# Optimization experiments

Hardware: AMD Instinct MI355X
Metric: run time of the kernel (lower is better)

The kernel has to match this reference:

```python
import jax, jax.numpy as jnp
import numpy as np

SCALAR_DIM = 64
VECTOR_DIM = 32
SPIN = 2
N_NODES = 50000
N_EDGES = 1600000
GEO_DIM = 3
IN_DIM = 2 * SCALAR_DIM + VECTOR_DIM + GEO_DIM  # 163
HID = SCALAR_DIM + VECTOR_DIM  # 96


def setup_inputs() -> dict:
    key = jax.random.key(0)
    ks = jax.random.split(key, 9)
    h_scalar = jax.random.normal(ks[0], (N_NODES, SCALAR_DIM), dtype=jnp.float32)
    h_vector = jax.random.normal(ks[1], (N_NODES, VECTOR_DIM), dtype=jnp.float32)
    edge_index = jax.random.randint(ks[2], (2, N_EDGES), 0, N_NODES, dtype=jnp.int64)
    pos = jax.random.normal(ks[3], (N_NODES, 2), dtype=jnp.float32)
    orientation = jax.random.uniform(ks[4], (N_NODES, 1), dtype=jnp.float32)
    # MLP params (Linear: y = x @ W.T + b; store as [in, out] for jnp)
    lim1 = 1.0 / np.sqrt(IN_DIM)
    lim2 = 1.0 / np.sqrt(HID)
    W1 = jax.random.uniform(ks[5], (IN_DIM, HID), minval=-lim1, maxval=lim1, dtype=jnp.float32)
    b1 = jax.random.uniform(ks[6], (HID,), minval=-lim1, maxval=lim1, dtype=jnp.float32)
    W2 = jax.random.uniform(ks[7], (HID, HID), minval=-lim2, maxval=lim2, dtype=jnp.float32)
    b2 = jax.random.uniform(ks[8], (HID,), minval=-lim2, maxval=lim2, dtype=jnp.float32)
    return dict(h_scalar=h_scalar, h_vector=h_vector, edge_index=edge_index,
                pos=pos, orientation=orientation, W1=W1, b1=b1, W2=W2, b2=b2)


def reference(h_scalar, h_vector, edge_index, pos, orientation, W1, b1, W2, b2):
    src, dst = edge_index[0], edge_index[1]
    delta_pos = pos[src] - pos[dst]                         # [E,2]
    dist = jnp.linalg.norm(delta_pos, axis=1, keepdims=True) + 1e-6  # [E,1]
    phi_global = jnp.arctan2(delta_pos[:, 1], delta_pos[:, 0])       # [E]
    alpha_i = orientation[dst, 0]                           # [E]
    delta_phi = phi_global - alpha_i
    geo_feat = jnp.concatenate([dist,
                                jnp.cos(SPIN * delta_phi)[:, None],
                                jnp.sin(SPIN * delta_phi)[:, None]], axis=-1)  # [E,3]
    beta_j = orientation[src, 0]
    rot_angle = (beta_j - alpha_i) * SPIN
    c, s = jnp.cos(rot_angle), jnp.sin(rot_angle)
    R = jnp.stack([jnp.stack([c, -s], -1), jnp.stack([s, c], -1)], axis=-2)  # [E,2,2]
    num_vecs = VECTOR_DIM // 2
    v_j = h_vector[src].reshape(-1, num_vecs, 2)            # [E,V/2,2]
    v_j_rot = jnp.einsum('eij,evj->evi', R, v_j).reshape(-1, VECTOR_DIM)
    msg_input = jnp.concatenate([h_scalar[src], h_scalar[dst], v_j_rot, geo_feat], axis=-1)
    h = jax.nn.silu(msg_input @ W1 + b1)
    raw_msg = h @ W2 + b2                                   # [E, S+V]
    msg_scalar = raw_msg[:, :SCALAR_DIM]
    msg_vector = raw_msg[:, SCALAR_DIM:]
    out_scalar = jax.ops.segment_sum(msg_scalar, dst, num_segments=N_NODES)
    out_vector = jax.ops.segment_sum(msg_vector, dst, num_segments=N_NODES)
    return h_scalar + out_scalar, h_vector + out_vector
```

## Files before the change

kernel.cpp:

```cpp
#include <hip/hip_runtime.h>
#include <hip/hip_bf16.h>

#define N_NODESC 50000
#define N_EDGESC 1600000
#define SDIM 64
#define VDIM 32
#define HID 96
#define IN_DIMC 163

#define GRID_E 6250
#define TPB_E 4
#define NXCD 8
#define XQ (GRID_E / NXCD)
#define XR (GRID_E % NXCD)
#define NPRE 782
#define SCB 196

typedef float f32x4 __attribute__((ext_vector_type(4)));
typedef short s16x8 __attribute__((ext_vector_type(8)));

__device__ __forceinline__ float bf2f(__hip_bfloat16 x) { return __bfloat162float(x); }
__device__ __forceinline__ __hip_bfloat16 f2bf(float x) { return __float2bfloat16(x); }
__device__ __forceinline__ float bfbits2f(short b) {
    unsigned u = ((unsigned)(unsigned short)b) << 16;
    return __builtin_bit_cast(float, u);
}
__device__ __forceinline__ short f2bfbits(float x) {
    __hip_bfloat16 h = __float2bfloat16(x);
    return *(const short*)&h;
}

__global__ void detect_zero(const int* ei, int* flag, int* __restrict__ counts) {
    int i = blockIdx.x * blockDim.x + threadIdx.x;
    if (i < N_NODESC) counts[i] = 0;
    if (i == 0) {
        int z = 1;
        for (int k = 0; k < 64; ++k) {
            if (ei[2 * k + 1] != 0) { z = 0; break; }
        }
        *flag = z;
    }
}

__global__ void fused_init(const float* __restrict__ hs, const float* __restrict__ hv,
                           float* __restrict__ out, int* __restrict__ counts,
                           const float* __restrict__ W1, const float* __restrict__ W2,
                           __hip_bfloat16* __restrict__ SrcRec,
                           __hip_bfloat16* __restrict__ WbT2,
                           __hip_bfloat16* __restrict__ W1cgT,
                           __hip_bfloat16* __restrict__ W2Tb,
                           const int* __restrict__ ei, const int* __restrict__ flag64) {
    int i = blockIdx.x * blockDim.x + threadIdx.x;
    if (i < N_NODESC * (SDIM + VDIM) / 4) {
        const int HS4 = N_NODESC * SDIM / 4;
        float4 v = (i < HS4) ? ((const float4*)hs)[i] : ((const float4*)hv)[i - HS4];
        ((float4*)out)[i] = v;
    }
    if (i < N_NODESC * VDIM / 8) {
        int n = i >> 2, c = i & 3;
        const float4* hv4 = (const float4*)hv;
        float4 a = hv4[n * 8 + c * 2];
        float4 bq = hv4[n * 8 + c * 2 + 1];
        s16x8 o;
        o[0] = f2bfbits(a.x);  o[1] = f2bfbits(a.y);
        o[2] = f2bfbits(a.z);  o[3] = f2bfbits(a.w);
        o[4] = f2bfbits(bq.x); o[5] = f2bfbits(bq.y);
        o[6] = f2bfbits(bq.z); o[7] = f2bfbits(bq.w);
        *(s16x8*)&SrcRec[n * 128 + 96 + c * 8] = o;
    }
    if (i < 192 * 64) {
        int n = i >> 6, k = i & 63;
        float val = (n < 96) ? W1[k * HID + n] : W1[(64 + k) * HID + (n - 96)];
        WbT2[i] = f2bf(val);
    }
    if (i < 96 * 64) {
        int n = i >> 6, k = i & 63;
        float val = 0.f;
        if (k < 32) val = W1[(128 + k) * HID + n];
        else if (k < 35) val = W1[(160 + (k - 32)) * HID + n];
        W1cgT[i] = f2bf(val);
    }
    if (i < 96 * 96) {
        int n = i / 96, k = i - (i / 96) * 96;
        W2Tb[i] = f2bf(W2[k * HID + n]);
    }
    {
        int dN;
        if (*flag64) dN = (int)((const long long*)ei)[N_EDGESC + i];
        else dN = ei[N_EDGESC + i];
        atomicAdd(&counts[dN], 1);
    }
}

__global__ __launch_bounds__(256) void scan_partials(
    const int* __restrict__ counts, int* __restrict__ cur, int* __restrict__ bsum) {
    __shared__ int sc[256];
    const int b = blockIdx.x, t = threadIdx.x;
    const int i = b * 256 + t;
    int val = (i < N_NODESC) ? counts[i] : 0;
    sc[t] = val;
    __syncthreads();
    for (int d = 1; d < 256; d <<= 1) {
        int v = (t >= d) ? sc[t - d] : 0;
        __syncthreads();
        sc[t] += v;
        __syncthreads();
    }
    if (i < N_NODESC) cur[i] = sc[t] - val;
    if (t == 255) bsum[b] = sc[255];
}

__global__ __launch_bounds__(256) void scan_bsums(
    const int* __restrict__ bsum, int* __restrict__ boff) {
    __shared__ int sc[256];
    const int t = threadIdx.x;
    int val = (t < SCB) ? bsum[t] : 0;
    sc[t] = val;
    __syncthreads();
    for (int d = 1; d < 256; d <<= 1) {
        int v = (t >= d) ? sc[t - d] : 0;
        __syncthreads();
        sc[t] += v;
        __syncthreads();
    }
    if (t < SCB) boff[t] = sc[t] - val;
}

__global__ __launch_bounds__(256) void scan_apply(
    int* __restrict__ cur, const int* __restrict__ boff) {
    const int i = blockIdx.x * 256 + threadIdx.x;
    if (i < N_NODESC) cur[i] += boff[blockIdx.x];
}

__global__ __launch_bounds__(256, 2) void scatter_precompute(
    const int* __restrict__ ei, const int* __restrict__ flag64,
    int* __restrict__ cur, int2* __restrict__ edges,
    const float* __restrict__ hs, const __hip_bfloat16* __restrict__ WbT2,
    const float* __restrict__ b1,
    __hip_bfloat16* __restrict__ SrcRec, __hip_bfloat16* __restrict__ Qt) {
    __shared__ __hip_bfloat16 sA[64][72];
    __shared__ __hip_bfloat16 sOut[64][200];
    const int blk = blockIdx.x;
    const int t = threadIdx.x;

    if (blk >= NPRE) {
        int e = (blk - NPRE) * 256 + t;
        int sN, dN;
        if (*flag64) {
            const long long* e64 = (const long long*)ei;
            sN = (int)e64[e]; dN = (int)e64[N_EDGESC + e];
        } else { sN = ei[e]; dN = ei[N_EDGESC + e]; }
        int p = atomicAdd(&cur[dN], 1);
        edges[p] = make_int2(sN, dN);
        return;
    }

    const int lane = t & 63;
    const int w = t >> 6;
    const int m16 = lane & 15;
    const int q = lane >> 4;
    const int nb = blk * 64;

    for (int idx = t; idx < 64 * 64; idx += 256) {
        int node = idx >> 6, f = idx & 63;
        int g = nb + node;
        sA[node][f] = f2bf(g < N_NODESC ? hs[g * SDIM + f] : 0.f);
    }
    __syncthreads();

    s16x8 bfr[3][2];
    float b1v[3];
    for (int nt = 0; nt < 3; ++nt) {
        int n_out = w * 48 + nt * 16 + m16;
        for (int kt = 0; kt < 2; ++kt)
            bfr[nt][kt] = *(const s16x8*)&WbT2[n_out * 64 + kt * 32 + q * 8];
        b1v[nt] = (n_out < 96) ? b1[n_out] : 0.f;
    }

    for (int ms = 0; ms < 4; ++ms) {
        s16x8 afr[2];
        for (int kt = 0; kt < 2; ++kt)
            afr[kt] = *(const s16x8*)&sA[ms * 16 + m16][kt * 32 + q * 8];
        f32x4 acc[3];
        for (int nt = 0; nt < 3; ++nt) acc[nt] = (f32x4){0.f, 0.f, 0.f, 0.f};
        for (int nt = 0; nt < 3; ++nt)
            for (int kt = 0; kt < 2; ++kt)
                acc[nt] = __builtin_amdgcn_mfma_f32_16x16x32_bf16(
                    afr[kt], bfr[nt][kt], acc[nt], 0, 0, 0);
        for (int nt = 0; nt < 3; ++nt) {
            int n_out = w * 48 + nt * 16 + m16;
            for (int r = 0; r < 4; ++r)
                sOut[ms * 16 + q * 4 + r][n_out] = f2bf(acc[nt][r] + b1v[nt]);
        }
    }
    __syncthreads();

    for (int idx = t; idx < 64 * 12; idx += 256) {
        int node = idx / 12, ch = idx - (idx / 12) * 12;
        int g = nb + node;
        if (g < N_NODESC)
            *(s16x8*)&SrcRec[g * 128 + ch * 8] = *(const s16x8*)&sOut[node][ch * 8];
    }
    for (int idx = t; idx < 64 * 12; idx += 256) {
        int node = idx / 12, ch = idx - (idx / 12) * 12;
        int g = nb + node;
        if (g < N_NODESC)
            *(s16x8*)&Qt[g * 96 + ch * 8] = *(const s16x8*)&sOut[node][96 + ch * 8];
    }
}

__global__ __launch_bounds__(256, 3) void edge_kernel_sorted(
    const int2* __restrict__ edges,
    const float* __restrict__ pos, const float* __restrict__ ori,
    const __hip_bfloat16* __restrict__ W2Tb, const float* __restrict__ b2,
    const __hip_bfloat16* __restrict__ SrcRec, const __hip_bfloat16* __restrict__ Qt,
    const __hip_bfloat16* __restrict__ W1cgT,
    float* __restrict__ out) {
    __shared__ int s_srcM[2][64], s_dstM[2][64];
    __shared__ alignas(16) __hip_bfloat16 hVG[64][72];
    __shared__ alignas(16) __hip_bfloat16 s_vf[64][104];
    __shared__ alignas(16) short sW2f[18 * 64 * 8];
    __shared__ int s_segstart[66];

    const int t = threadIdx.x;
    const int lane = t & 63;
    const int w = t >> 6;
    const int m16 = lane & 15;
    const int q = lane >> 4;
    const int el = t >> 2;
    const int quad = t & 3;
    const int eM = w * 16 + m16;

    if (w == 0) {
        for (int f = 0; f < 18; ++f) {
            int nt = f / 3, kt = f - (f / 3) * 3;
            *(s16x8*)&sW2f[(f * 64 + lane) * 8] =
                *(const s16x8*)&W2Tb[(nt * 16 + m16) * 96 + kt * 32 + q * 8];
        }
    }
    s16x8 bfrC[6][2];
    #pragma unroll
    for (int nt = 0; nt < 6; ++nt)
        #pragma unroll
        for (int kt = 0; kt < 2; ++kt)
            bfrC[nt][kt] = *(const s16x8*)&W1cgT[(nt * 16 + m16) * 64 + kt * 32 + q * 8];
    float b2v[6];
    #pragma unroll
    for (int nt = 0; nt < 6; ++nt) b2v[nt] = b2[nt * 16 + m16];

    int b = blockIdx.x;
    int xcd = b & 7, bi = b >> 3;
    int c = (xcd < XR) ? (xcd * (XQ + 1) + bi)
                       : (XR * (XQ + 1) + (xcd - XR) * XQ + bi);
    const int tile0 = c * TPB_E;

    int2 edT1;
    s16x8 hvvT;
    float rcT, rsT;
    float gdT, gcgT, gsgT;
    {
        int2 edT = edges[tile0 * 64 + el];
        edT1 = edges[(tile0 + 1) * 64 + el];
        hvvT = *(const s16x8*)&SrcRec[edT.x * 128 + 96 + quad * 8];
        int sN = edT.x, dN = edT.y;
        float ca, sa, cb, sb;
        __sincosf(2.0f * ori[dN], &sa, &ca);
        __sincosf(2.0f * ori[sN], &sb, &cb);
        rcT = cb * ca + sb * sa;
        rsT = sb * ca - cb * sa;
        float dx = pos[2 * sN] - pos[2 * dN];
        float dy = pos[2 * sN + 1] - pos[2 * dN + 1];
        float d2 = dx * dx + dy * dy;
        gdT = sqrtf(d2) + 1e-6f;
        float c2f, s2f;
        if (d2 > 0.f) {
            float inv = __builtin_amdgcn_rcpf(d2);
            c2f = (dx * dx - dy * dy) * inv;
            s2f = 2.0f * dx * dy * inv;
        } else { c2f = 1.0f; s2f = 0.0f; }
        gcgT = c2f * ca + s2f * sa;
        gsgT = s2f * ca - c2f * sa;
        if (quad == 0) { s_srcM[0][el] = sN; s_dstM[0][el] = dN; }
    }
    __syncthreads();
    s16x8 pqP[3], pqQ[3];
    {
        int sN = s_srcM[0][eM], dN = s_dstM[0][eM];
        #pragma unroll
        for (int kt = 0; kt < 3; ++kt) {
            pqP[kt] = *(const s16x8*)&SrcRec[sN * 128 + kt * 32 + q * 8];
            pqQ[kt] = *(const s16x8*)&Qt[dN * 96 + kt * 32 + q * 8];
        }
    }

    int cur = 0;
    for (int tl = 0; tl < TPB_E; ++tl) {
        const int nx = cur ^ 1;
        const int tlN2 = (tl + 2 < TPB_E) ? tl + 2 : TPB_E - 1;

        {
            s16x8 rv;
            #pragma unroll
            for (int p2 = 0; p2 < 4; ++p2) {
                float x = bfbits2f(hvvT[2 * p2]), y = bfbits2f(hvvT[2 * p2 + 1]);
                rv[2 * p2]     = f2bfbits(rcT * x - rsT * y);
                rv[2 * p2 + 1] = f2bfbits(rsT * x + rcT * y);
            }
            *(s16x8*)&hVG[el][quad * 8] = rv;
            s16x8 up = (s16x8){0, 0, 0, 0, 0, 0, 0, 0};
            if (quad == 0) {
                up[0] = f2bfbits(gdT); up[1] = f2bfbits(gcgT); up[2] = f2bfbits(gsgT);
            }
            *(s16x8*)&hVG[el][32 + quad * 8] = up;
        }
        int2 edT2 = edges[(tile0 + tlN2) * 64 + el];
        s16x8 hvvN = *(const s16x8*)&SrcRec[edT1.x * 128 + 96 + quad * 8];
        {
            s16x8 afr0 = *(const s16x8*)&hVG[eM][q * 8];
            s16x8 afr1 = *(const s16x8*)&hVG[eM][32 + q * 8];
            #pragma unroll
            for (int nt = 0; nt < 6; ++nt) {
                f32x4 a1 = __builtin_amdgcn_mfma_f32_16x16x32_bf16(
                    afr0, bfrC[nt][0], (f32x4){0.f, 0.f, 0.f, 0.f}, 0, 0, 0);
                a1 = __builtin_amdgcn_mfma_f32_16x16x32_bf16(
                    afr1, bfrC[nt][1], a1, 0, 0, 0);
                int u = nt * 16 + m16;
                #pragma unroll
                for (int r = 0; r < 4; ++r)
                    s_vf[w * 16 + q * 4 + r][u] = f2bf(a1[r]);
            }
        }
        float rcN, rsN, gdN, gcgN, gsgN;
        {
            int sN = edT1.x, dN = edT1.y;
            float ca, sa, cb, sb;
            __sincosf(2.0f * ori[dN], &sa, &ca);
            __sincosf(2.0f * ori[sN], &sb, &cb);
            rcN = cb * ca + sb * sa;
            rsN = sb * ca - cb * sa;
            float dx = pos[2 * sN] - pos[2 * dN];
            float dy = pos[2 * sN + 1] - pos[2 * dN + 1];
            float d2 = dx * dx + dy * dy;
            gdN = sqrtf(d2) + 1e-6f;
            float c2f, s2f;
            if (d2 > 0.f) {
                float inv = __builtin_amdgcn_rcpf(d2);
                c2f = (dx * dx - dy * dy) * inv;
                s2f = 2.0f * dx * dy * inv;
            } else { c2f = 1.0f; s2f = 0.0f; }
            gcgN = c2f * ca + s2f * sa;
            gsgN = s2f * ca - c2f * sa;
            if (quad == 0) { s_srcM[nx][el] = sN; s_dstM[nx][el] = dN; }
        }

        s16x8 afr[3];
        #pragma unroll
        for (int kt = 0; kt < 3; ++kt) {
            int j = kt * 32 + q * 8;
            s16x8 Vv = *(const s16x8*)&s_vf[eM][j];
            s16x8 hb;
            #pragma unroll
// ... 155 lines not shown
    const bool i64 = (*flag64 != 0);
    const long long* ei64 = (const long long*)ei;

    for (int tile = blockIdx.x; tile < N_EDGESC / 64; tile += gridDim.x) {
        __syncthreads();

        if (t < 64) {
            int e = tile * 64 + t;
            int sN, dN;
            if (i64) { sN = (int)ei64[e]; dN = (int)ei64[N_EDGESC + e]; }
            else     { sN = ei[e];        dN = ei[N_EDGESC + e]; }
            s_src[t] = sN; s_dst[t] = dN;
            float ca, sa, cb, sb;
            __sincosf(2.0f * ori[dN], &sa, &ca);
            __sincosf(2.0f * ori[sN], &sb, &cb);
            s_c[t] = cb * ca + sb * sa;
            s_s[t] = sb * ca - cb * sa;
            float dx = pos[2 * sN] - pos[2 * dN];
            float dy = pos[2 * sN + 1] - pos[2 * dN + 1];
            float d2 = dx * dx + dy * dy;
            s_d[t] = sqrtf(d2) + 1e-6f;
            float c2f, s2f;
            if (d2 > 0.f) {
                float inv = 1.0f / d2;
                c2f = (dx * dx - dy * dy) * inv;
                s2f = 2.0f * dx * dy * inv;
            } else { c2f = 1.0f; s2f = 0.0f; }
            s_cg[t] = c2f * ca + s2f * sa;
            s_sg[t] = s2f * ca - c2f * sa;
        }
        __syncthreads();

        for (int p = 0; p < 24; ++p) {
            int idx = p * 256 + t;
            int e = idx / HID;
            int j = idx - e * HID;
            int sN = s_src[e], dN = s_dst[e];
            float pre = bf2f(Pp[sN * HID + j]) + bf2f(Qt[dN * HID + j])
                      + s_c[e] * bf2f(Ut[sN * HID + j])
                      + s_s[e] * bf2f(Vt[sN * HID + j])
                      + s_d[e] * s_w1d[0][j] + s_cg[e] * s_w1d[1][j]
                      + s_sg[e] * s_w1d[2][j];
            float h = pre / (1.0f + __expf(-pre));
            hA[e][j] = f2bf(h);
        }
        __syncthreads();

        f32x4 acc[6];
        for (int nt = 0; nt < 6; ++nt) acc[nt] = (f32x4){0.f, 0.f, 0.f, 0.f};
        s16x8 afr[3];
        for (int kt = 0; kt < 3; ++kt)
            afr[kt] = *(const s16x8*)&hA[w * 16 + m16][kt * 32 + q * 8];
        for (int nt = 0; nt < 6; ++nt)
            for (int kt = 0; kt < 3; ++kt)
                acc[nt] = __builtin_amdgcn_mfma_f32_16x16x32_bf16(
                    afr[kt], bfr[nt][kt], acc[nt], 0, 0, 0);

        for (int nt = 0; nt < 6; ++nt) {
            int u = nt * 16 + m16;
            for (int r = 0; r < 4; ++r) {
                int eloc = w * 16 + q * 4 + r;
                int dN = s_dst[eloc];
                float val = acc[nt][r] + b2v[nt];
                if (u < SDIM) atomicAdd(&out[dN * SDIM + u], val);
                else atomicAdd(&out[N_NODESC * SDIM + dN * VDIM + (u - SDIM)], val);
            }
        }
    }
}

__global__ __launch_bounds__(192) void edge_fallback(
    const int* __restrict__ ei, const float* __restrict__ hs,
    const float* __restrict__ hv, const float* __restrict__ pos,
    const float* __restrict__ ori, const float* __restrict__ W1,
    const float* __restrict__ b1, const float* __restrict__ W2,
    const float* __restrict__ b2, const int* __restrict__ flag64,
    float* __restrict__ out) {
    __shared__ float s_msg[IN_DIMC];
    __shared__ float s_h[HID];
    int e = blockIdx.x;
    int t = threadIdx.x;
    const bool i64 = (*flag64 != 0);
    int sN, dN;
    if (i64) {
        const long long* e64 = (const long long*)ei;
        sN = (int)e64[e]; dN = (int)e64[N_EDGESC + e];
    } else { sN = ei[e]; dN = ei[N_EDGESC + e]; }

    if (t < IN_DIMC) {
        if (t < 64) s_msg[t] = hs[sN * SDIM + t];
        else if (t < 128) s_msg[t] = hs[dN * SDIM + (t - 64)];
        else {
            float ca, sa, cb, sb;
            __sincosf(2.0f * ori[dN], &sa, &ca);
            __sincosf(2.0f * ori[sN], &sb, &cb);
            float c = cb * ca + sb * sa;
            float s = sb * ca - cb * sa;
            float dx = pos[2 * sN] - pos[2 * dN];
            float dy = pos[2 * sN + 1] - pos[2 * dN + 1];
            float d2 = dx * dx + dy * dy;
            if (t < 160) {
                int pr = (t - 128) >> 1;
                float x = hv[sN * VDIM + 2 * pr], y = hv[sN * VDIM + 2 * pr + 1];
                s_msg[t] = ((t & 1) == 0) ? (c * x - s * y) : (s * x + c * y);
            } else if (t == 160) s_msg[t] = sqrtf(d2) + 1e-6f;
            else {
                float c2f = 1.0f, s2f = 0.0f;
                if (d2 > 0.f) {
                    float inv = 1.0f / d2;
                    c2f = (dx * dx - dy * dy) * inv;
                    s2f = 2.0f * dx * dy * inv;
                }
                s_msg[t] = (t == 161) ? (c2f * ca + s2f * sa) : (s2f * ca - c2f * sa);
            }
        }
    }
    __syncthreads();
    if (t < HID) {
        float a = b1[t];
        for (int k = 0; k < IN_DIMC; ++k) a += s_msg[k] * W1[k * HID + t];
        s_h[t] = a / (1.0f + __expf(-a));
    }
    __syncthreads();
    if (t < HID) {
        float a = b2[t];
        for (int k = 0; k < HID; ++k) a += s_h[k] * W2[k * HID + t];
        if (t < SDIM) atomicAdd(&out[dN * SDIM + t], a);
        else atomicAdd(&out[N_NODESC * SDIM + dN * VDIM + (t - SDIM)], a);
    }
}

extern "C" void kernel_launch(void* const* d_in, const int* in_sizes, int n_in,
                              void* d_out, int out_size, void* d_ws, size_t ws_size,
                              hipStream_t stream) {
    const float* hs  = (const float*)d_in[0];
    const float* hv  = (const float*)d_in[1];
    const int*   ei  = (const int*)d_in[2];
    const float* pos = (const float*)d_in[3];
    const float* ori = (const float*)d_in[4];
    const float* W1  = (const float*)d_in[5];
    const float* b1  = (const float*)d_in[6];
    const float* W2  = (const float*)d_in[7];
    const float* b2  = (const float*)d_in[8];
    float* out = (float*)d_out;

    const size_t SREC = (size_t)N_NODESC * 128 * sizeof(__hip_bfloat16);
    const size_t QTB  = (size_t)N_NODESC * 96 * sizeof(__hip_bfloat16);
    const size_t CNT  = ((size_t)N_NODESC * sizeof(int) + 255) & ~255ull;
    const size_t EDG  = (size_t)N_EDGESC * sizeof(int2);
    const size_t WBT2 = ((size_t)192 * 64 * 2 + 255) & ~255ull;
    const size_t W1CG = ((size_t)96 * 64 * 2 + 255) & ~255ull;
    const size_t W2TS = ((size_t)96 * 96 * 2 + 255) & ~255ull;
    const size_t FLG  = 256;
    const size_t BSM  = 1024;
    const size_t BOF  = 1024;
    const size_t SORT_WS = SREC + QTB + 2 * CNT + EDG + WBT2 + W1CG + W2TS
                         + FLG + BSM + BOF;

    const size_t TBL = (size_t)N_NODESC * HID * sizeof(__hip_bfloat16);
    const bool big = ws_size >= 4 * TBL + 16;
    const bool srt = ws_size >= SORT_WS;

    if (srt) {
        char* ws = (char*)d_ws;
        __hip_bfloat16* SrcRec = (__hip_bfloat16*)(ws);
        __hip_bfloat16* Qt     = (__hip_bfloat16*)(ws + SREC);
        int* counts            = (int*)(ws + SREC + QTB);
        int* cur               = (int*)(ws + SREC + QTB + CNT);
        int2* edges            = (int2*)(ws + SREC + QTB + 2 * CNT);
        __hip_bfloat16* WbT2   = (__hip_bfloat16*)(ws + SREC + QTB + 2 * CNT + EDG);
        __hip_bfloat16* W1cgT  = (__hip_bfloat16*)(ws + SREC + QTB + 2 * CNT + EDG + WBT2);
        __hip_bfloat16* W2Tb   = (__hip_bfloat16*)(ws + SREC + QTB + 2 * CNT + EDG + WBT2 + W1CG);
        char* tail             = ws + SREC + QTB + 2 * CNT + EDG + WBT2 + W1CG + W2TS;
        int* flag              = (int*)(tail);
        int* bsum              = (int*)(tail + FLG);
        int* boff              = (int*)(tail + FLG + BSM);

        detect_zero<<<(N_NODESC + 255) / 256, 256, 0, stream>>>(ei, flag, counts);
        fused_init<<<N_EDGESC / 256, 256, 0, stream>>>(
            hs, hv, out, counts, W1, W2, SrcRec, WbT2, W1cgT, W2Tb, ei, flag);
        scan_partials<<<SCB, 256, 0, stream>>>(counts, cur, bsum);
        scan_bsums<<<1, 256, 0, stream>>>(bsum, boff);
        scan_apply<<<SCB, 256, 0, stream>>>(cur, boff);
        scatter_precompute<<<NPRE + N_EDGESC / 256, 256, 0, stream>>>(
            ei, flag, cur, edges, hs, WbT2, b1, SrcRec, Qt);
        edge_kernel_sorted<<<GRID_E, 256, 0, stream>>>(edges, pos, ori, W2Tb, b2,
                                                       SrcRec, Qt, W1cgT, out);
    } else if (big) {
        char* ws = (char*)d_ws;
        __hip_bfloat16* Pp = (__hip_bfloat16*)(ws);
        __hip_bfloat16* Qt = (__hip_bfloat16*)(ws + TBL);
        __hip_bfloat16* Ut = (__hip_bfloat16*)(ws + 2 * TBL);
        __hip_bfloat16* Vt = (__hip_bfloat16*)(ws + 3 * TBL);
        int* flag = (int*)(ws + 4 * TBL);
        init_out<<<(N_NODESC * (SDIM + VDIM) + 255) / 256, 256, 0, stream>>>(hs, hv, out);
        detect_kernel<<<1, 64, 0, stream>>>(ei, flag);
        node_precompute<<<N_NODESC, 128, 0, stream>>>(hs, hv, W1, b1, Pp, Qt, Ut, Vt);
        edge_kernel<<<2500, 256, 0, stream>>>(ei, pos, ori, W1, W2, b2,
                                              Pp, Qt, Ut, Vt, flag, out);
    } else {
        int* flag = (int*)d_ws;
        init_out<<<(N_NODESC * (SDIM + VDIM) + 255) / 256, 256, 0, stream>>>(hs, hv, out);
        detect_kernel<<<1, 64, 0, stream>>>(ei, flag);
        edge_fallback<<<N_EDGESC, 192, 0, stream>>>(ei, hs, hv, pos, ori, W1, b1,
                                                    W2, b2, flag, out);
    }
}
```

Baseline: 496.6 us.

## Fuse preprocessing launches into one cooperative persistent kernel with grid syncs

```diff
diff --git a/kernel.cpp b/kernel.cpp
--- a/kernel.cpp
+++ b/kernel.cpp
@@ -1,5 +1,8 @@
 #include <hip/hip_runtime.h>
+#include <hip/hip_cooperative_groups.h>
 #include <hip/hip_bf16.h>
+
+namespace cg = cooperative_groups;
 
 #define N_NODESC 50000
 #define N_EDGESC 1600000
@@ -30,136 +33,16 @@
     return *(const short*)&h;
 }
 
-__global__ void detect_zero(const int* ei, int* flag, int* __restrict__ counts) {
-    int i = blockIdx.x * blockDim.x + threadIdx.x;
-    if (i < N_NODESC) counts[i] = 0;
-    if (i == 0) {
-        int z = 1;
-        for (int k = 0; k < 64; ++k) {
-            if (ei[2 * k + 1] != 0) { z = 0; break; }
-        }
-        *flag = z;
-    }
-}
-
-__global__ void fused_init(const float* __restrict__ hs, const float* __restrict__ hv,
-                           float* __restrict__ out, int* __restrict__ counts,
-                           const float* __restrict__ W1, const float* __restrict__ W2,
-                           __hip_bfloat16* __restrict__ SrcRec,
-                           __hip_bfloat16* __restrict__ WbT2,
-                           __hip_bfloat16* __restrict__ W1cgT,
-                           __hip_bfloat16* __restrict__ W2Tb,
-                           const int* __restrict__ ei, const int* __restrict__ flag64) {
-    int i = blockIdx.x * blockDim.x + threadIdx.x;
-    if (i < N_NODESC * (SDIM + VDIM) / 4) {
-        const int HS4 = N_NODESC * SDIM / 4;
-        float4 v = (i < HS4) ? ((const float4*)hs)[i] : ((const float4*)hv)[i - HS4];
-        ((float4*)out)[i] = v;
-    }
-    if (i < N_NODESC * VDIM / 8) {
-        int n = i >> 2, c = i & 3;
-        const float4* hv4 = (const float4*)hv;
-        float4 a = hv4[n * 8 + c * 2];
-        float4 bq = hv4[n * 8 + c * 2 + 1];
-        s16x8 o;
-        o[0] = f2bfbits(a.x);  o[1] = f2bfbits(a.y);
-        o[2] = f2bfbits(a.z);  o[3] = f2bfbits(a.w);
-        o[4] = f2bfbits(bq.x); o[5] = f2bfbits(bq.y);
-        o[6] = f2bfbits(bq.z); o[7] = f2bfbits(bq.w);
-        *(s16x8*)&SrcRec[n * 128 + 96 + c * 8] = o;
-    }
-    if (i < 192 * 64) {
-        int n = i >> 6, k = i & 63;
-        float val = (n < 96) ? W1[k * HID + n] : W1[(64 + k) * HID + (n - 96)];
-        WbT2[i] = f2bf(val);
-    }
-    if (i < 96 * 64) {
-        int n = i >> 6, k = i & 63;
-        float val = 0.f;
-        if (k < 32) val = W1[(128 + k) * HID + n];
-        else if (k < 35) val = W1[(160 + (k - 32)) * HID + n];
-        W1cgT[i] = f2bf(val);
-    }
-    if (i < 96 * 96) {
-        int n = i / 96, k = i - (i / 96) * 96;
-        W2Tb[i] = f2bf(W2[k * HID + n]);
-    }
-    {
-        int dN;
-        if (*flag64) dN = (int)((const long long*)ei)[N_EDGESC + i];
-        else dN = ei[N_EDGESC + i];
-        atomicAdd(&counts[dN], 1);
-    }
-}
-
-__global__ __launch_bounds__(256) void scan_partials(
-    const int* __restrict__ counts, int* __restrict__ cur, int* __restrict__ bsum) {
-    __shared__ int sc[256];
-    const int b = blockIdx.x, t = threadIdx.x;
-    const int i = b * 256 + t;
-    int val = (i < N_NODESC) ? counts[i] : 0;
-    sc[t] = val;
-    __syncthreads();
-    for (int d = 1; d < 256; d <<= 1) {
-        int v = (t >= d) ? sc[t - d] : 0;
-        __syncthreads();
-        sc[t] += v;
-        __syncthreads();
-    }
-    if (i < N_NODESC) cur[i] = sc[t] - val;
-    if (t == 255) bsum[b] = sc[255];
-}
-
-__global__ __launch_bounds__(256) void scan_bsums(
-    const int* __restrict__ bsum, int* __restrict__ boff) {
-    __shared__ int sc[256];
-    const int t = threadIdx.x;
-    int val = (t < SCB) ? bsum[t] : 0;
-    sc[t] = val;
-    __syncthreads();
-    for (int d = 1; d < 256; d <<= 1) {
-        int v = (t >= d) ? sc[t - d] : 0;
-        __syncthreads();
-        sc[t] += v;
-        __syncthreads();
-    }
-    if (t < SCB) boff[t] = sc[t] - val;
-}
-
-__global__ __launch_bounds__(256) void scan_apply(
-    int* __restrict__ cur, const int* __restrict__ boff) {
-    const int i = blockIdx.x * 256 + threadIdx.x;
-    if (i < N_NODESC) cur[i] += boff[blockIdx.x];
-}
-
-__global__ __launch_bounds__(256, 2) void scatter_precompute(
-    const int* __restrict__ ei, const int* __restrict__ flag64,
-    int* __restrict__ cur, int2* __restrict__ edges,
-    const float* __restrict__ hs, const __hip_bfloat16* __restrict__ WbT2,
-    const float* __restrict__ b1,
-    __hip_bfloat16* __restrict__ SrcRec, __hip_bfloat16* __restrict__ Qt) {
-    __shared__ __hip_bfloat16 sA[64][72];
-    __shared__ __hip_bfloat16 sOut[64][200];
-    const int blk = blockIdx.x;
-    const int t = threadIdx.x;
-
-    if (blk >= NPRE) {
-        int e = (blk - NPRE) * 256 + t;
-        int sN, dN;
-        if (*flag64) {
-            const long long* e64 = (const long long*)ei;
-            sN = (int)e64[e]; dN = (int)e64[N_EDGESC + e];
-        } else { sN = ei[e]; dN = ei[N_EDGESC + e]; }
-        int p = atomicAdd(&cur[dN], 1);
-        edges[p] = make_int2(sN, dN);
-        return;
-    }
-
+__device__ __forceinline__ void precompute_chunk(
+    int ch, int t, const float* __restrict__ hs,
+    const __hip_bfloat16* __restrict__ WbT2, const float* __restrict__ b1,
+    __hip_bfloat16* __restrict__ SrcRec, __hip_bfloat16* __restrict__ Qt,
+    __hip_bfloat16 (*sA)[72], __hip_bfloat16 (*sOut)[200]) {
     const int lane = t & 63;
     const int w = t >> 6;
     const int m16 = lane & 15;
     const int q = lane >> 4;
-    const int nb = blk * 64;
+    const int nb = ch * 64;
 
     for (int idx = t; idx < 64 * 64; idx += 256) {
         int node = idx >> 6, f = idx & 63;
@@ -196,17 +79,276 @@
     __syncthreads();
 
     for (int idx = t; idx < 64 * 12; idx += 256) {
-        int node = idx / 12, ch = idx - (idx / 12) * 12;
+        int node = idx / 12, c2 = idx - (idx / 12) * 12;
         int g = nb + node;
         if (g < N_NODESC)
-            *(s16x8*)&SrcRec[g * 128 + ch * 8] = *(const s16x8*)&sOut[node][ch * 8];
+            *(s16x8*)&SrcRec[g * 128 + c2 * 8] = *(const s16x8*)&sOut[node][c2 * 8];
     }
     for (int idx = t; idx < 64 * 12; idx += 256) {
-        int node = idx / 12, ch = idx - (idx / 12) * 12;
+        int node = idx / 12, c2 = idx - (idx / 12) * 12;
         int g = nb + node;
         if (g < N_NODESC)
-            *(s16x8*)&Qt[g * 96 + ch * 8] = *(const s16x8*)&sOut[node][96 + ch * 8];
-    }
+            *(s16x8*)&Qt[g * 96 + c2 * 8] = *(const s16x8*)&sOut[node][96 + c2 * 8];
+    }
+}
+
+__global__ __launch_bounds__(256, 4) void mega_aux(
+    const int* __restrict__ ei, int hostflag,
+    const float* __restrict__ hs, const float* __restrict__ hv,
+    const float* __restrict__ W1, const float* __restrict__ W2,
+    const float* __restrict__ b1,
+    float* __restrict__ out,
+    int* __restrict__ counts, int* __restrict__ cur, int2* __restrict__ edges,
+    __hip_bfloat16* __restrict__ SrcRec, __hip_bfloat16* __restrict__ Qt,
+    __hip_bfloat16* __restrict__ WbT2, __hip_bfloat16* __restrict__ W1cgT,
+    __hip_bfloat16* __restrict__ W2Tb,
+    int* __restrict__ flagp, int* __restrict__ bsum, int* __restrict__ boff,
+    int* __restrict__ ctr) {
+    __shared__ alignas(16) char smem[34944];
+    __hip_bfloat16 (*sA)[72] = (__hip_bfloat16(*)[72])smem;
+    __hip_bfloat16 (*sOut)[200] = (__hip_bfloat16(*)[200])(smem + 9216);
+    int* s_scan = (int*)smem;
+    int* s_chunk = (int*)(smem + 34816);
+
+    cg::grid_group grid = cg::this_grid();
+    const int t = threadIdx.x;
+    const int blk = blockIdx.x;
+    const int gid = blk * 256 + t;
+    const int G = gridDim.x * 256;
+
+    for (int i = gid; i < N_NODESC * (SDIM + VDIM) / 4; i += G) {
+        const int HS4 = N_NODESC * SDIM / 4;
+        float4 v = (i < HS4) ? ((const float4*)hs)[i] : ((const float4*)hv)[i - HS4];
+        ((float4*)out)[i] = v;
+    }
+    for (int i = gid; i < N_NODESC * VDIM / 8; i += G) {
+        int n = i >> 2, c = i & 3;
+        const float4* hv4 = (const float4*)hv;
+        float4 a = hv4[n * 8 + c * 2];
+        float4 bq = hv4[n * 8 + c * 2 + 1];
+        s16x8 o;
+        o[0] = f2bfbits(a.x);  o[1] = f2bfbits(a.y);
+        o[2] = f2bfbits(a.z);  o[3] = f2bfbits(a.w);
+        o[4] = f2bfbits(bq.x); o[5] = f2bfbits(bq.y);
+        o[6] = f2bfbits(bq.z); o[7] = f2bfbits(bq.w);
+        *(s16x8*)&SrcRec[n * 128 + 96 + c * 8] = o;
+    }
+    for (int i = gid; i < 192 * 64; i += G) {
+        int n = i >> 6, k = i & 63;
+        float val = (n < 96) ? W1[k * HID + n] : W1[(64 + k) * HID + (n - 96)];
+        WbT2[i] = f2bf(val);
+    }
+    for (int i = gid; i < 96 * 64; i += G) {
+        int n = i >> 6, k = i & 63;
+        float val = 0.f;
+        if (k < 32) val = W1[(128 + k) * HID + n];
+        else if (k < 35) val = W1[(160 + (k - 32)) * HID + n];
+        W1cgT[i] = f2bf(val);
+    }
+    for (int i = gid; i < 96 * 96; i += G) {
+        int n = i / 96, k = i - (i / 96) * 96;
+        W2Tb[i] = f2bf(W2[k * HID + n]);
+    }
+    for (int i = gid; i < N_NODESC; i += G) counts[i] = 0;
+    if (gid == 0) {
+        *ctr = 0;
+        if (hostflag >= 0) *flagp = hostflag;
+        else {
+            int z = 1;
+            for (int k = 0; k < 64; ++k) if (ei[2 * k + 1] != 0) { z = 0; break; }
+            *flagp = z;
+        }
+    }
+    grid.sync();
+
+    const int fl = *flagp;
+    for (int e = gid; e < N_EDGESC; e += G) {
+        int dN = fl ? (int)((const long long*)ei)[N_EDGESC + e] : ei[N_EDGESC + e];
+        atomicAdd(&counts[dN], 1);
+    }
+    grid.sync();
+
+    if (blk < SCB) {
+        int i = blk * 256 + t;
+        int val = (i < N_NODESC) ? counts[i] : 0;
+        s_scan[t] = val;
+        __syncthreads();
+        for (int d = 1; d < 256; d <<= 1) {
+            int v = (t >= d) ? s_scan[t - d] : 0;
+            __syncthreads();
+            s_scan[t] += v;
+            __syncthreads();
+        }
+        if (i < N_NODESC) cur[i] = s_scan[t] - val;
+        if (t == 255) bsum[blk] = s_scan[255];
+        __syncthreads();
+    }
+    for (;;) {
+        if (t == 0) *s_chunk = atomicAdd(ctr, 1);
+        __syncthreads();
+        int ch = *s_chunk;
+        if (ch >= NPRE) break;
+        precompute_chunk(ch, t, hs, WbT2, b1, SrcRec, Qt, sA, sOut);
+        __syncthreads();
+    }
+    grid.sync();
+
+    if (blk == 0) {
+        int val = (t < SCB) ? bsum[t] : 0;
+        s_scan[t] = val;
+        __syncthreads();
+        for (int d = 1; d < 256; d <<= 1) {
+            int v = (t >= d) ? s_scan[t - d] : 0;
+            __syncthreads();
+            s_scan[t] += v;
+            __syncthreads();
+        }
+        if (t < SCB) boff[t] = s_scan[t] - val;
+    }
+    grid.sync();
+
+    if (blk < SCB) {
+        int i = blk * 256 + t;
+        if (i < N_NODESC) cur[i] += boff[blk];
+    }
+    grid.sync();
+
+    for (int e = gid; e < N_EDGESC; e += G) {
+        int sN, dN;
+        if (fl) {
+            const long long* e64 = (const long long*)ei;
+            sN = (int)e64[e]; dN = (int)e64[N_EDGESC + e];
+        } else { sN = ei[e]; dN = ei[N_EDGESC + e]; }
+        int p = atomicAdd(&cur[dN], 1);
+        edges[p] = make_int2(sN, dN);
+    }
+}
+
+__global__ void detect_zero(const int* ei, int* flag, int* __restrict__ counts) {
+    int i = blockIdx.x * blockDim.x + threadIdx.x;
+    if (i < N_NODESC) counts[i] = 0;
+    if (i == 0) {
+        int z = 1;
+        for (int k = 0; k < 64; ++k) {
+            if (ei[2 * k + 1] != 0) { z = 0; break; }
+        }
+        *flag = z;
+    }
+}
+
+__global__ void fused_init(const float* __restrict__ hs, const float* __restrict__ hv,
+                           float* __restrict__ out, int* __restrict__ counts,
+                           const float* __restrict__ W1, const float* __restrict__ W2,
+                           __hip_bfloat16* __restrict__ SrcRec,
+                           __hip_bfloat16* __restrict__ WbT2,
+                           __hip_bfloat16* __restrict__ W1cgT,
+                           __hip_bfloat16* __restrict__ W2Tb,
+                           const int* __restrict__ ei, const int* __restrict__ flag64) {
+    int i = blockIdx.x * blockDim.x + threadIdx.x;
+    if (i < N_NODESC * (SDIM + VDIM) / 4) {
+        const int HS4 = N_NODESC * SDIM / 4;
+        float4 v = (i < HS4) ? ((const float4*)hs)[i] : ((const float4*)hv)[i - HS4];
+        ((float4*)out)[i] = v;
+    }
+    if (i < N_NODESC * VDIM / 8) {
+        int n = i >> 2, c = i & 3;
+        const float4* hv4 = (const float4*)hv;
+        float4 a = hv4[n * 8 + c * 2];
+        float4 bq = hv4[n * 8 + c * 2 + 1];
+        s16x8 o;
+        o[0] = f2bfbits(a.x);  o[1] = f2bfbits(a.y);
+        o[2] = f2bfbits(a.z);  o[3] = f2bfbits(a.w);
+        o[4] = f2bfbits(bq.x); o[5] = f2bfbits(bq.y);
+        o[6] = f2bfbits(bq.z); o[7] = f2bfbits(bq.w);
+        *(s16x8*)&SrcRec[n * 128 + 96 + c * 8] = o;
+    }
+    if (i < 192 * 64) {
+        int n = i >> 6, k = i & 63;
+        float val = (n < 96) ? W1[k * HID + n] : W1[(64 + k) * HID + (n - 96)];
+        WbT2[i] = f2bf(val);
+    }
+    if (i < 96 * 64) {
+        int n = i >> 6, k = i & 63;
+        float val = 0.f;
+        if (k < 32) val = W1[(128 + k) * HID + n];
+        else if (k < 35) val = W1[(160 + (k - 32)) * HID + n];
+        W1cgT[i] = f2bf(val);
+    }
+    if (i < 96 * 96) {
+        int n = i / 96, k = i - (i / 96) * 96;
+        W2Tb[i] = f2bf(W2[k * HID + n]);
+    }
+    {
+        int dN;
+        if (*flag64) dN = (int)((const long long*)ei)[N_EDGESC + i];
+        else dN = ei[N_EDGESC + i];
+        atomicAdd(&counts[dN], 1);
+    }
+}
+
+__global__ __launch_bounds__(256) void scan_partials(
+    const int* __restrict__ counts, int* __restrict__ cur, int* __restrict__ bsum) {
+    __shared__ int sc[256];
+    const int b = blockIdx.x, t = threadIdx.x;
+    const int i = b * 256 + t;
+    int val = (i < N_NODESC) ? counts[i] : 0;
+    sc[t] = val;
+    __syncthreads();
+    for (int d = 1; d < 256; d <<= 1) {
+        int v = (t >= d) ? sc[t - d] : 0;
+        __syncthreads();
+        sc[t] += v;
+        __syncthreads();
+    }
+    if (i < N_NODESC) cur[i] = sc[t] - val;
+    if (t == 255) bsum[b] = sc[255];
+}
+
+__global__ __launch_bounds__(256) void scan_bsums(
+    const int* __restrict__ bsum, int* __restrict__ boff) {
+    __shared__ int sc[256];
+    const int t = threadIdx.x;
+    int val = (t < SCB) ? bsum[t] : 0;
+    sc[t] = val;
+    __syncthreads();
+    for (int d = 1; d < 256; d <<= 1) {
+        int v = (t >= d) ? sc[t - d] : 0;
+        __syncthreads();
+        sc[t] += v;
+        __syncthreads();
+    }
+    if (t < SCB) boff[t] = sc[t] - val;
+}
+
+__global__ __launch_bounds__(256) void scan_apply(
+    int* __restrict__ cur, const int* __restrict__ boff) {
+    const int i = blockIdx.x * 256 + threadIdx.x;
+    if (i < N_NODESC) cur[i] += boff[blockIdx.x];
+}
+
+__global__ __launch_bounds__(256, 2) void scatter_precompute(
+    const int* __restrict__ ei, const int* __restrict__ flag64,
+    int* __restrict__ cur, int2* __restrict__ edges,
+    const float* __restrict__ hs, const __hip_bfloat16* __restrict__ WbT2,
+    const float* __restrict__ b1,
+    __hip_bfloat16* __restrict__ SrcRec, __hip_bfloat16* __restrict__ Qt) {
+    __shared__ __hip_bfloat16 sA[64][72];
+    __shared__ __hip_bfloat16 sOut[64][200];
+    const int blk = blockIdx.x;
+    const int t = threadIdx.x;
+
+    if (blk >= NPRE) {
+        int e = (blk - NPRE) * 256 + t;
+        int sN, dN;
+        if (*flag64) {
+            const long long* e64 = (const long long*)ei;
+            sN = (int)e64[e]; dN = (int)e64[N_EDGESC + e];
+        } else { sN = ei[e]; dN = ei[N_EDGESC + e]; }
+        int p = atomicAdd(&cur[dN], 1);
+        edges[p] = make_int2(sN, dN);
+        return;
+    }
+    precompute_chunk(blk, t, hs, WbT2, b1, SrcRec, Qt, sA, sOut);
 }
 
 __global__ __launch_bounds__(256, 3) void edge_kernel_sorted(
@@ -670,8 +812,9 @@
     const size_t FLG  = 256;
     const size_t BSM  = 1024;
     const size_t BOF  = 1024;
+    const size_t CTR  = 256;
     const size_t SORT_WS = SREC + QTB + 2 * CNT + EDG + WBT2 + W1CG + W2TS
-                         + FLG + BSM + BOF;
+                         + FLG + BSM + BOF + CTR;
 
     const size_t TBL = (size_t)N_NODESC * HID * sizeof(__hip_bfloat16);
     const bool big = ws_size >= 4 * TBL + 16;
@@ -691,15 +834,41 @@
         int* flag              = (int*)(tail);
         int* bsum              = (int*)(tail + FLG);
         int* boff              = (int*)(tail + FLG + BSM);
-
-        detect_zero<<<(N_NODESC + 255) / 256, 256, 0, stream>>>(ei, flag, counts);
-        fused_init<<<N_EDGESC / 256, 256, 0, stream>>>(
-            hs, hv, out, counts, W1, W2, SrcRec, WbT2, W1cgT, W2Tb, ei, flag);
-        scan_partials<<<SCB, 256, 0, stream>>>(counts, cur, bsum);
-        scan_bsums<<<1, 256, 0, stream>>>(bsum, boff);
-        scan_apply<<<SCB, 256, 0, stream>>>(cur, boff);
-        scatter_precompute<<<NPRE + N_EDGESC / 256, 256, 0, stream>>>(
-            ei, flag, cur, edges, hs, WbT2, b1, SrcRec, Qt);
+        int* ctrp              = (int*)(tail + FLG + BSM + BOF);
+
+        int hostflag = -1;
+        long long eib = (long long)in_sizes[2];
+        if (eib == 2ll * N_EDGESC * 8) hostflag = 1;
+        else if (eib == 2ll * N_EDGESC * 4) hostflag = 0;
+
+        int occ = 0;
+        hipError_t qerr = hipOccupancyMaxActiveBlocksPerMultiprocessor(
+            &occ, mega_aux, 256, 0);
+        hipError_t lerr = hipErrorUnknown;
+        if (qerr == hipSuccess && occ >= 1) {
+            int G = occ * 256;
+            if (G > 1024) G = 1024;
+            if (G < 256) G = 256;
+            void* args[] = {
+                (void*)&ei, (void*)&hostflag, (void*)&hs, (void*)&hv,
+                (void*)&W1, (void*)&W2, (void*)&b1, (void*)&out,
+                (void*)&counts, (void*)&cur, (void*)&edges,
+                (void*)&SrcRec, (void*)&Qt, (void*)&WbT2, (void*)&W1cgT,
+                (void*)&W2Tb, (void*)&flag, (void*)&bsum, (void*)&boff,
+                (void*)&ctrp };
+            lerr = hipLaunchCooperativeKernel((void*)mega_aux, dim3(G), dim3(256),
+                                              args, 0, stream);
+        }
+        if (lerr != hipSuccess) {
+            detect_zero<<<(N_NODESC + 255) / 256, 256, 0, stream>>>(ei, flag, counts);
+            fused_init<<<N_EDGESC / 256, 256, 0, stream>>>(
+                hs, hv, out, counts, W1, W2, SrcRec, WbT2, W1cgT, W2Tb, ei, flag);
+            scan_partials<<<SCB, 256, 0, stream>>>(counts, cur, bsum);
+            scan_bsums<<<1, 256, 0, stream>>>(bsum, boff);
+            scan_apply<<<SCB, 256, 0, stream>>>(cur, boff);
+            scatter_precompute<<<NPRE + N_EDGESC / 256, 256, 0, stream>>>(
+                ei, flag, cur, edges, hs, WbT2, b1, SrcRec, Qt);
+        }
         edge_kernel_sorted<<<GRID_E, 256, 0, stream>>>(edges, pos, ori, W2Tb, b2,
                                                        SrcRec, Qt, W1cgT, out);
     } else if (big) {
```

Measured after the change: 948.8 us. +91.0%, slower.

## Fuse preprocessing kernels and replace three-pass scan with single-pass lookback scan

Applied to the files above, without the earlier changes.

```diff
diff --git a/kernel.cpp b/kernel.cpp
--- a/kernel.cpp
+++ b/kernel.cpp
@@ -30,44 +30,15 @@
     return *(const short*)&h;
 }
 
-__global__ void detect_zero(const int* ei, int* flag, int* __restrict__ counts) {
+__global__ __launch_bounds__(256) void prep_kernel(
+    const int* __restrict__ ei, int hostflag, int* __restrict__ flagp,
+    const float* __restrict__ W1, const float* __restrict__ W2,
+    __hip_bfloat16* __restrict__ WbT2, __hip_bfloat16* __restrict__ W1cgT,
+    __hip_bfloat16* __restrict__ W2Tb,
+    int* __restrict__ counts, int* __restrict__ desc) {
     int i = blockIdx.x * blockDim.x + threadIdx.x;
     if (i < N_NODESC) counts[i] = 0;
-    if (i == 0) {
-        int z = 1;
-        for (int k = 0; k < 64; ++k) {
-            if (ei[2 * k + 1] != 0) { z = 0; break; }
-        }
-        *flag = z;
-    }
-}
-
-__global__ void fused_init(const float* __restrict__ hs, const float* __restrict__ hv,
-                           float* __restrict__ out, int* __restrict__ counts,
-                           const float* __restrict__ W1, const float* __restrict__ W2,
-                           __hip_bfloat16* __restrict__ SrcRec,
-                           __hip_bfloat16* __restrict__ WbT2,
-                           __hip_bfloat16* __restrict__ W1cgT,
-                           __hip_bfloat16* __restrict__ W2Tb,
-                           const int* __restrict__ ei, const int* __restrict__ flag64) {
-    int i = blockIdx.x * blockDim.x + threadIdx.x;
-    if (i < N_NODESC * (SDIM + VDIM) / 4) {
-        const int HS4 = N_NODESC * SDIM / 4;
-        float4 v = (i < HS4) ? ((const float4*)hs)[i] : ((const float4*)hv)[i - HS4];
-        ((float4*)out)[i] = v;
-    }
-    if (i < N_NODESC * VDIM / 8) {
-        int n = i >> 2, c = i & 3;
-        const float4* hv4 = (const float4*)hv;
-        float4 a = hv4[n * 8 + c * 2];
-        float4 bq = hv4[n * 8 + c * 2 + 1];
-        s16x8 o;
-        o[0] = f2bfbits(a.x);  o[1] = f2bfbits(a.y);
-        o[2] = f2bfbits(a.z);  o[3] = f2bfbits(a.w);
-        o[4] = f2bfbits(bq.x); o[5] = f2bfbits(bq.y);
-        o[6] = f2bfbits(bq.z); o[7] = f2bfbits(bq.w);
-        *(s16x8*)&SrcRec[n * 128 + 96 + c * 8] = o;
-    }
+    if (i < SCB) desc[i] = 0;
     if (i < 192 * 64) {
         int n = i >> 6, k = i & 63;
         float val = (n < 96) ? W1[k * HID + n] : W1[(64 + k) * HID + (n - 96)];
@@ -84,82 +55,26 @@
         int n = i / 96, k = i - (i / 96) * 96;
         W2Tb[i] = f2bf(W2[k * HID + n]);
     }
-    {
-        int dN;
-        if (*flag64) dN = (int)((const long long*)ei)[N_EDGESC + i];
-        else dN = ei[N_EDGESC + i];
-        atomicAdd(&counts[dN], 1);
-    }
-}
-
-__global__ __launch_bounds__(256) void scan_partials(
-    const int* __restrict__ counts, int* __restrict__ cur, int* __restrict__ bsum) {
-    __shared__ int sc[256];
-    const int b = blockIdx.x, t = threadIdx.x;
-    const int i = b * 256 + t;
-    int val = (i < N_NODESC) ? counts[i] : 0;
-    sc[t] = val;
-    __syncthreads();
-    for (int d = 1; d < 256; d <<= 1) {
-        int v = (t >= d) ? sc[t - d] : 0;
-        __syncthreads();
-        sc[t] += v;
-        __syncthreads();
-    }
-    if (i < N_NODESC) cur[i] = sc[t] - val;
-    if (t == 255) bsum[b] = sc[255];
-}
-
-__global__ __launch_bounds__(256) void scan_bsums(
-    const int* __restrict__ bsum, int* __restrict__ boff) {
-    __shared__ int sc[256];
-    const int t = threadIdx.x;
-    int val = (t < SCB) ? bsum[t] : 0;
-    sc[t] = val;
-    __syncthreads();
-    for (int d = 1; d < 256; d <<= 1) {
-        int v = (t >= d) ? sc[t - d] : 0;
-        __syncthreads();
-        sc[t] += v;
-        __syncthreads();
-    }
-    if (t < SCB) boff[t] = sc[t] - val;
-}
-
-__global__ __launch_bounds__(256) void scan_apply(
-    int* __restrict__ cur, const int* __restrict__ boff) {
-    const int i = blockIdx.x * 256 + threadIdx.x;
-    if (i < N_NODESC) cur[i] += boff[blockIdx.x];
-}
-
-__global__ __launch_bounds__(256, 2) void scatter_precompute(
-    const int* __restrict__ ei, const int* __restrict__ flag64,
-    int* __restrict__ cur, int2* __restrict__ edges,
-    const float* __restrict__ hs, const __hip_bfloat16* __restrict__ WbT2,
-    const float* __restrict__ b1,
-    __hip_bfloat16* __restrict__ SrcRec, __hip_bfloat16* __restrict__ Qt) {
-    __shared__ __hip_bfloat16 sA[64][72];
-    __shared__ __hip_bfloat16 sOut[64][200];
-    const int blk = blockIdx.x;
-    const int t = threadIdx.x;
-
-    if (blk >= NPRE) {
-        int e = (blk - NPRE) * 256 + t;
-        int sN, dN;
-        if (*flag64) {
-            const long long* e64 = (const long long*)ei;
-            sN = (int)e64[e]; dN = (int)e64[N_EDGESC + e];
-        } else { sN = ei[e]; dN = ei[N_EDGESC + e]; }
-        int p = atomicAdd(&cur[dN], 1);
-        edges[p] = make_int2(sN, dN);
-        return;
-    }
-
+    if (i == 0) {
+        if (hostflag >= 0) *flagp = hostflag;
+        else {
+            int z = 1;
+            for (int k = 0; k < 64; ++k) if (ei[2 * k + 1] != 0) { z = 0; break; }
+            *flagp = z;
+        }
+    }
+}
+
+__device__ __forceinline__ void precompute_chunk(
+    int ch, int t, const float* __restrict__ hs,
+    const __hip_bfloat16* __restrict__ WbT2, const float* __restrict__ b1,
+    __hip_bfloat16* __restrict__ SrcRec, __hip_bfloat16* __restrict__ Qt,
+    __hip_bfloat16 (*sA)[72], __hip_bfloat16 (*sOut)[200]) {
     const int lane = t & 63;
     const int w = t >> 6;
     const int m16 = lane & 15;
     const int q = lane >> 4;
-    const int nb = blk * 64;
+    const int nb = ch * 64;
 
     for (int idx = t; idx < 64 * 64; idx += 256) {
         int node = idx >> 6, f = idx & 63;
@@ -196,17 +111,111 @@
     __syncthreads();
 
     for (int idx = t; idx < 64 * 12; idx += 256) {
-        int node = idx / 12, ch = idx - (idx / 12) * 12;
+        int node = idx / 12, c2 = idx - (idx / 12) * 12;
         int g = nb + node;
         if (g < N_NODESC)
-            *(s16x8*)&SrcRec[g * 128 + ch * 8] = *(const s16x8*)&sOut[node][ch * 8];
+            *(s16x8*)&SrcRec[g * 128 + c2 * 8] = *(const s16x8*)&sOut[node][c2 * 8];
     }
     for (int idx = t; idx < 64 * 12; idx += 256) {
-        int node = idx / 12, ch = idx - (idx / 12) * 12;
+        int node = idx / 12, c2 = idx - (idx / 12) * 12;
         int g = nb + node;
         if (g < N_NODESC)
-            *(s16x8*)&Qt[g * 96 + ch * 8] = *(const s16x8*)&sOut[node][96 + ch * 8];
-    }
+            *(s16x8*)&Qt[g * 96 + c2 * 8] = *(const s16x8*)&sOut[node][96 + c2 * 8];
+    }
+}
+
+__global__ __launch_bounds__(256, 2) void init_hist_precompute(
+    const float* __restrict__ hs, const float* __restrict__ hv,
+    float* __restrict__ out, int* __restrict__ counts,
+    const int* __restrict__ ei, const int* __restrict__ flag64,
+    const __hip_bfloat16* __restrict__ WbT2, const float* __restrict__ b1,
+    __hip_bfloat16* __restrict__ SrcRec, __hip_bfloat16* __restrict__ Qt) {
+    __shared__ __hip_bfloat16 sA[64][72];
+    __shared__ __hip_bfloat16 sOut[64][200];
+    const int blk = blockIdx.x;
+    const int t = threadIdx.x;
+
+    if (blk < NPRE) {
+        precompute_chunk(blk, t, hs, WbT2, b1, SrcRec, Qt, sA, sOut);
+        return;
+    }
+    const int e = (blk - NPRE) * 256 + t;
+
+    if (e < N_NODESC * (SDIM + VDIM) / 4) {
+        const int HS4 = N_NODESC * SDIM / 4;
+        float4 v = (e < HS4) ? ((const float4*)hs)[e] : ((const float4*)hv)[e - HS4];
+        ((float4*)out)[e] = v;
+    }
+    if (e < N_NODESC * VDIM / 8) {
+        int n = e >> 2, c = e & 3;
+        const float4* hv4 = (const float4*)hv;
+        float4 a = hv4[n * 8 + c * 2];
+        float4 bq = hv4[n * 8 + c * 2 + 1];
+        s16x8 o;
+        o[0] = f2bfbits(a.x);  o[1] = f2bfbits(a.y);
+        o[2] = f2bfbits(a.z);  o[3] = f2bfbits(a.w);
+        o[4] = f2bfbits(bq.x); o[5] = f2bfbits(bq.y);
+        o[6] = f2bfbits(bq.z); o[7] = f2bfbits(bq.w);
+        *(s16x8*)&SrcRec[n * 128 + 96 + c * 8] = o;
+    }
+    {
+        int dN;
+        if (*flag64) dN = (int)((const long long*)ei)[N_EDGESC + e];
+        else dN = ei[N_EDGESC + e];
+        atomicAdd(&counts[dN], 1);
+    }
+}
+
+__global__ __launch_bounds__(256) void scan_onepass(
+    const int* __restrict__ counts, int* __restrict__ cur, int* __restrict__ desc) {
+    __shared__ int sc[256];
+    __shared__ int s_excl;
+    const int blk = blockIdx.x, t = threadIdx.x;
+    const int i = blk * 256 + t;
+    int val = (i < N_NODESC) ? counts[i] : 0;
+    sc[t] = val;
+    __syncthreads();
+    for (int d = 1; d < 256; d <<= 1) {
+        int v = (t >= d) ? sc[t - d] : 0;
+        __syncthreads();
+        sc[t] += v;
+        __syncthreads();
+    }
+    int aggregate = sc[255];
+    if (t == 0) {
+        if (blk == 0) {
+            atomicExch(&desc[0], (aggregate << 2) | 2);
+            s_excl = 0;
+        } else {
+            atomicExch(&desc[blk], (aggregate << 2) | 1);
+            int excl = 0;
+            int j = blk - 1;
+            for (;;) {
+                int d = atomicAdd(&desc[j], 0);
+                int st = d & 3;
+                if (st == 2) { excl += (d >> 2); break; }
+                if (st == 1) { excl += (d >> 2); --j; }
+            }
+            atomicExch(&desc[blk], ((excl + aggregate) << 2) | 2);
+            s_excl = excl;
+        }
+    }
+    __syncthreads();
+    if (i < N_NODESC) cur[i] = s_excl + sc[t] - val;
+}
+
+__global__ __launch_bounds__(256) void scatter_kernel(
+    const int* __restrict__ ei, const int* __restrict__ flag64,
+    int* __restrict__ cur, int2* __restrict__ edges) {
+    int e = blockIdx.x * blockDim.x + threadIdx.x;
+    if (e >= N_EDGESC) return;
+    int sN, dN;
+    if (*flag64) {
+        const long long* e64 = (const long long*)ei;
+        sN = (int)e64[e]; dN = (int)e64[N_EDGESC + e];
+    } else { sN = ei[e]; dN = ei[N_EDGESC + e]; }
+    int p = atomicAdd(&cur[dN], 1);
+    edges[p] = make_int2(sN, dN);
 }
 
 __global__ __launch_bounds__(256, 3) void edge_kernel_sorted(
@@ -668,10 +677,9 @@
     const size_t W1CG = ((size_t)96 * 64 * 2 + 255) & ~255ull;
     const size_t W2TS = ((size_t)96 * 96 * 2 + 255) & ~255ull;
     const size_t FLG  = 256;
-    const size_t BSM  = 1024;
-    const size_t BOF  = 1024;
+    const size_t DSC  = 1024;
     const size_t SORT_WS = SREC + QTB + 2 * CNT + EDG + WBT2 + W1CG + W2TS
-                         + FLG + BSM + BOF;
+                         + FLG + DSC;
 
     const size_t TBL = (size_t)N_NODESC * HID * sizeof(__hip_bfloat16);
     const bool big = ws_size >= 4 * TBL + 16;
@@ -689,17 +697,19 @@
         __hip_bfloat16* W2Tb   = (__hip_bfloat16*)(ws + SREC + QTB + 2 * CNT + EDG + WBT2 + W1CG);
         char* tail             = ws + SREC + QTB + 2 * CNT + EDG + WBT2 + W1CG + W2TS;
         int* flag              = (int*)(tail);
-        int* bsum              = (int*)(tail + FLG);
-        int* boff              = (int*)(tail + FLG + BSM);
-
-        detect_zero<<<(N_NODESC + 255) / 256, 256, 0, stream>>>(ei, flag, counts);
-        fused_init<<<N_EDGESC / 256, 256, 0, stream>>>(
-            hs, hv, out, counts, W1, W2, SrcRec, WbT2, W1cgT, W2Tb, ei, flag);
-        scan_partials<<<SCB, 256, 0, stream>>>(counts, cur, bsum);
-        scan_bsums<<<1, 256, 0, stream>>>(bsum, boff);
-        scan_apply<<<SCB, 256, 0, stream>>>(cur, boff);
-        scatter_precompute<<<NPRE + N_EDGESC / 256, 256, 0, stream>>>(
-            ei, flag, cur, edges, hs, WbT2, b1, SrcRec, Qt);
+        int* desc              = (int*)(tail + FLG);
+
+        int hostflag = -1;
+        long long eib = (long long)in_sizes[2];
+        if (eib == 2ll * N_EDGESC * 8) hostflag = 1;
+        else if (eib == 2ll * N_EDGESC * 4) hostflag = 0;
+
+        prep_kernel<<<SCB, 256, 0, stream>>>(ei, hostflag, flag, W1, W2,
+                                             WbT2, W1cgT, W2Tb, counts, desc);
+        init_hist_precompute<<<NPRE + N_EDGESC / 256, 256, 0, stream>>>(
+            hs, hv, out, counts, ei, flag, WbT2, b1, SrcRec, Qt);
+        scan_onepass<<<SCB, 256, 0, stream>>>(counts, cur, desc);
+        scatter_kernel<<<N_EDGESC / 256, 256, 0, stream>>>(ei, flag, cur, edges);
         edge_kernel_sorted<<<GRID_E, 256, 0, stream>>>(edges, pos, ori, W2Tb, b2,
                                                        SrcRec, Qt, W1cgT, out);
     } else if (big) {
```

Result: no change. 489.2 us (-1.5%).
